# Kernel tuning notes

Hardware: AMD Instinct MI355X
Metric: run time of the kernel (lower is better)

## Reference

```python
import jax, jax.numpy as jnp
import numpy as np

WAY = 5
SHOT = 5
SCALE = 10.0
EPS = 1e-8


def setup_inputs() -> dict:
    key = jax.random.key(0)
    k1, k2 = jax.random.split(key, 2)
    x = jax.random.normal(k1, (100, 512, 16, 16), dtype=jnp.float32)
    W = jax.random.normal(k2, (512, 512), dtype=jnp.float32) * 0.02  # 1x1 conv weight (outC, inC)
    b = jnp.zeros((512,), dtype=jnp.float32)
    return {"x": x, "W": W, "b": b}


def reference(x, W, b):
    B, C, H, Wd = x.shape
    # extract(): 1x1 conv -> softmax over flattened (C*H*W) per sample -> remask
    mask = jnp.einsum('bchw,oc->bohw', x, W) + b[None, :, None, None]
    mask = jax.nn.softmax(mask.reshape(B, -1), axis=1).reshape(B, C, H, Wd)
    x = x * mask
    # predict(): (way, shot+query, C, H, W)
    xv = x.reshape(WAY, -1, C, H, Wd)
    s = xv[:, :SHOT].mean(axis=(1, 3, 4))                    # (m=way, d=C) support prototypes
    q = xv[:, SHOT:].reshape(-1, C, H * Wd)                  # (n, d=C, f=H*W) queries
    # cosine_similarity over d, without materializing (n,m,d,f)
    qn = jnp.maximum(jnp.sqrt(jnp.sum(q * q, axis=1)), EPS)  # (n, f)
    sn = jnp.maximum(jnp.sqrt(jnp.sum(s * s, axis=1)), EPS)  # (m,)
    scores = jnp.einsum('ndf,md->nmf', q, s) / (qn[:, None, :] * sn[None, :, None])
    # softmax over classes (m), then mean over spatial positions f
    return jax.nn.softmax(SCALE * scores, axis=1).mean(axis=2)  # (n, way)
```

## Files before the change

kernel.cpp:

```cpp
#include <hip/hip_runtime.h>
#include <hip/hip_bf16.h>
#include <math.h>

typedef _Float16 half8 __attribute__((ext_vector_type(8)));
typedef float f32x4 __attribute__((ext_vector_type(4)));

#define BATCH 100
#define CH    512
#define HWP   256
#define SAMP  (CH * HWP)

__device__ __forceinline__ void async16(const void* g, void* l) {
  __builtin_amdgcn_global_load_lds(
      (const __attribute__((address_space(1))) unsigned int*)g,
      (__attribute__((address_space(3))) unsigned int*)l, 16, 0, 0);
}

__global__ __launch_bounds__(256) void k_txpose(const float* __restrict__ x,
                                               _Float16* __restrict__ xh) {
  __shared__ float tb[64][69];
  int bid  = blockIdx.x;
  int b    = bid >> 5;
  int tile = bid & 31;
  int c0 = (tile >> 2) << 6;
  int p0 = (tile & 3) << 6;
  int t = threadIdx.x;
  const float* xb = x + (size_t)b * SAMP;
#pragma unroll
  for (int it = 0; it < 4; it++) {
    int ch = it * 256 + t;
    int c  = ch >> 4;
    int pc = (ch & 15) << 2;
    float4 v = *(const float4*)(xb + (size_t)(c0 + c) * HWP + p0 + pc);
    tb[c][pc] = v.x; tb[c][pc + 1] = v.y; tb[c][pc + 2] = v.z; tb[c][pc + 3] = v.w;
  }
  __syncthreads();
  _Float16* xhb = xh + (size_t)b * SAMP;
#pragma unroll
  for (int it = 0; it < 2; it++) {
    int ch = it * 256 + t;
    int p  = ch >> 3;
    int ck = (ch & 7) << 3;
    half8 h;
#pragma unroll
    for (int j = 0; j < 8; j++) h[j] = (_Float16)tb[ck + j][p];
    *(half8*)(xhb + (size_t)(p0 + p) * CH + c0 + ck) = h;
  }
}

__global__ __launch_bounds__(256) void k_convw(const float* __restrict__ W,
                                              _Float16* __restrict__ Wh) {
  int base = blockIdx.x * 1024 + threadIdx.x;
#pragma unroll
  for (int j = 0; j < 4; j++) Wh[base + j * 256] = (_Float16)W[base + j * 256];
}

__global__ __launch_bounds__(256) void k_gemm(const _Float16* __restrict__ Wh,
                                             const _Float16* __restrict__ xh,
                                             const float* __restrict__ bias,
                                             _Float16* __restrict__ u,
                                             float* __restrict__ denom) {
  __shared__ __align__(16) _Float16 smem[128 * 136];
  _Float16* As = smem;
  _Float16* Bs = smem + 4096;
  int bid   = blockIdx.x;
  int batch = bid >> 3;
  int sub   = bid & 7;
  int ot = sub & 3, pt = sub >> 2;
  int o0 = ot * 128, p0 = pt * 128;
  const _Float16* Bg = xh + (size_t)batch * SAMP;

  int t  = threadIdx.x;
  int wv = t >> 6, ln = t & 63;
  int qd = ln >> 4, r = ln & 15;
  int wm0 = (wv >> 1) * 64, wn0 = (wv & 1) * 64;

  f32x4 acc[4][4] = {};

  for (int kk = 0; kk < 512; kk += 32) {
#pragma unroll
    for (int it = 0; it < 2; it++) {
      int ch  = it * 256 + t;
      int row = ch >> 2;
      int qc  = ch & 3;
      char* la = (char*)As + (size_t)(it * 256 + wv * 64) * 16;
      char* lb = (char*)Bs + (size_t)(it * 256 + wv * 64) * 16;
      async16((const char*)(Wh + (size_t)(o0 + row) * 512 + kk + qc * 8), la);
      async16((const char*)(Bg + (size_t)(p0 + row) * 512 + kk + qc * 8), lb);
    }
    __syncthreads();
    half8 af[4], bf[4];
#pragma unroll
    for (int i = 0; i < 4; i++)
      af[i] = *(const half8*)(As + (wm0 + i * 16 + r) * 32 + qd * 8);
#pragma unroll
    for (int j = 0; j < 4; j++)
      bf[j] = *(const half8*)(Bs + (wn0 + j * 16 + r) * 32 + qd * 8);
#pragma unroll
    for (int i = 0; i < 4; i++)
#pragma unroll
      for (int j = 0; j < 4; j++)
        acc[i][j] = __builtin_amdgcn_mfma_f32_16x16x32_f16(af[i], bf[j], acc[i][j], 0, 0, 0);
    __syncthreads();
  }

#pragma unroll
  for (int it = 0; it < 8; it++) {
    int ch = it * 256 + t;
    int p  = ch >> 4;
    int ck = ch & 15;
    half8 v = *(const half8*)(Bg + (size_t)(p0 + p) * CH + o0 + ck * 8);
    *(half8*)(smem + p * 136 + ck * 8) = v;
  }
  __syncthreads();

  _Float16* outb = u + (size_t)batch * SAMP;
  float lsum = 0.f;
#pragma unroll
  for (int i = 0; i < 4; i++) {
#pragma unroll
    for (int rg = 0; rg < 4; rg++) {
      int ol = wm0 + i * 16 + qd * 4 + rg;
      float bv = bias[o0 + ol];
#pragma unroll
      for (int j = 0; j < 4; j++) {
        int pl = wn0 + j * 16 + r;
        float ev = __expf(acc[i][j][rg] + bv);
        lsum += ev;
        float xv = (float)smem[pl * 136 + ol];
        outb[(size_t)(o0 + ol) * HWP + p0 + pl] = (_Float16)(xv * ev);
      }
    }
  }
#pragma unroll
  for (int off = 32; off; off >>= 1) lsum += __shfl_down(lsum, off, 64);
  __shared__ float rs[4];
  if (ln == 0) rs[wv] = lsum;
  __syncthreads();
  if (t == 0) atomicAdd(&denom[batch], rs[0] + rs[1] + rs[2] + rs[3]);
}

__global__ __launch_bounds__(256) void k_proto(const _Float16* __restrict__ u,
                                              const float* __restrict__ denom,
                                              float* __restrict__ sproto) {
  int m = blockIdx.x / 512, c = blockIdx.x % 512;
  int t = threadIdx.x;
  float acc = 0.f;
  for (int j = 0; j < 5; j++) {
    int b = m * 20 + j;
    float invd = 1.0f / denom[b];
    acc += (float)u[(size_t)b * SAMP + (size_t)c * HWP + t] * invd;
  }
#pragma unroll
  for (int off = 32; off; off >>= 1) acc += __shfl_down(acc, off, 64);
  __shared__ float rs[4];
  if ((t & 63) == 0) rs[t >> 6] = acc;
  __syncthreads();
  if (t == 0) sproto[m * 512 + c] = (rs[0] + rs[1] + rs[2] + rs[3]) * (1.0f / 1280.0f);
}

__global__ __launch_bounds__(256) void k_sn(const float* __restrict__ sproto,
                                           float* __restrict__ pref) {
  int m = blockIdx.x, t = threadIdx.x;
  float v1 = sproto[m * 512 + t], v2 = sproto[m * 512 + 256 + t];
  float acc = v1 * v1 + v2 * v2;
#pragma unroll
  for (int off = 32; off; off >>= 1) acc += __shfl_down(acc, off, 64);
  __shared__ float rs[4];
  if ((t & 63) == 0) rs[t >> 6] = acc;
  __syncthreads();
  if (t == 0) {
    float sn = fmaxf(sqrtf(rs[0] + rs[1] + rs[2] + rs[3]), 1e-8f);
    pref[m] = 10.0f / sn;
  }
}

__global__ __launch_bounds__(256) void k_part(const _Float16* __restrict__ u,
                                             const float* __restrict__ sproto,
                                             float* __restrict__ part) {
  __shared__ float s_l[5 * 64];
  int n = blockIdx.x >> 3, gc = blockIdx.x & 7;
  int b = (n / 15) * 20 + 5 + (n % 15);
  int t = threadIdx.x;
  for (int i = t; i < 320; i += 256)
    s_l[i] = sproto[(i >> 6) * 512 + gc * 64 + (i & 63)];
  __syncthreads();
  const _Float16* ub = u + (size_t)b * SAMP + (size_t)gc * 64 * HWP;
  float dot[5] = {0, 0, 0, 0, 0}, qq = 0.f;
#pragma unroll 8
  for (int c = 0; c < 64; c++) {
    float v = (float)ub[c * HWP + t];
    qq += v * v;
#pragma unroll
    for (int m = 0; m < 5; m++) dot[m] += v * s_l[m * 64 + c];
  }
  float* pp = part + (((size_t)n * 8 + gc) * 256 + t) * 6;
  pp[0] = dot[0]; pp[1] = dot[1]; pp[2] = dot[2];
  pp[3] = dot[3]; pp[4] = dot[4]; pp[5] = qq;
}

__global__ __launch_bounds__(256) void k_comb(const float* __restrict__ part,
                                             const float* __restrict__ pref,
                                             float* __restrict__ out) {
  int n = blockIdx.x, t = threadIdx.x;
  float dot[5] = {0, 0, 0, 0, 0}, qq = 0.f;
#pragma unroll
  for (int gc = 0; gc < 8; gc++) {
    const float* pp = part + (((size_t)n * 8 + gc) * 256 + t) * 6;
    dot[0] += pp[0]; dot[1] += pp[1]; dot[2] += pp[2];
    dot[3] += pp[3]; dot[4] += pp[4]; qq += pp[5];
  }
  float iqn = 1.0f / fmaxf(sqrtf(qq), 1e-20f);
  float sc[5], mx = -1e30f;
#pragma unroll
  for (int m = 0; m < 5; m++) { sc[m] = dot[m] * pref[m] * iqn; mx = fmaxf(mx, sc[m]); }
  float p[5], ssum = 0.f;
#pragma unroll
  for (int m = 0; m < 5; m++) { p[m] = __expf(sc[m] - mx); ssum += p[m]; }
  float rr = 1.0f / ssum;
#pragma unroll
  for (int m = 0; m < 5; m++) {
    float v = p[m] * rr;
#pragma unroll
    for (int off = 32; off; off >>= 1) v += __shfl_down(v, off, 64);
    p[m] = v;
  }
  __shared__ float rs[4][5];
  if ((t & 63) == 0) {
#pragma unroll
    for (int m = 0; m < 5; m++) rs[t >> 6][m] = p[m];
  }
  __syncthreads();
  if (t < 5) out[n * 5 + t] =
      (rs[0][t] + rs[1][t] + rs[2][t] + rs[3][t]) * (1.0f / 256.0f);
}

extern "C" void kernel_launch(void* const* d_in, const int* in_sizes, int n_in,
                              void* d_out, int out_size, void* d_ws, size_t ws_size,
                              hipStream_t stream) {
  const float* x    = (const float*)d_in[0];
  const float* W    = (const float*)d_in[1];
  const float* bias = (const float*)d_in[2];
  float* out = (float*)d_out;

  char* ws = (char*)d_ws;
  _Float16* xh     = (_Float16*)(ws + 0);
  float*    part   = (float*)   (ws + 0);
  _Float16* Wh     = (_Float16*)(ws + 26214400);
  _Float16* u      = (_Float16*)(ws + 26738688);
  float*    denom  = (float*)   (ws + 52953088);
  float*    sproto = (float*)   (ws + 52953600);
  float*    pref   = (float*)   (ws + 52963840);

  hipMemsetAsync(denom, 0, 512, stream);
  k_txpose <<<3200, 256, 0, stream>>>(x, xh);
  k_convw  <<<256,  256, 0, stream>>>(W, Wh);
  k_gemm   <<<800,  256, 0, stream>>>(Wh, xh, bias, u, denom);
  k_proto  <<<2560, 256, 0, stream>>>(u, denom, sproto);
  k_sn     <<<5,    256, 0, stream>>>(sproto, pref);
  k_part   <<<600,  256, 0, stream>>>(u, sproto, part);
  k_comb   <<<75,   256, 0, stream>>>(part, pref, out);
}
```

Before: 142.1 us.

## Fuse small kernels and stage GEMM epilogue through LDS for coalesced stores

```diff
diff --git a/kernel.cpp b/kernel.cpp
--- a/kernel.cpp
+++ b/kernel.cpp
@@ -17,14 +17,22 @@
 }
 
 __global__ __launch_bounds__(256) void k_txpose(const float* __restrict__ x,
-                                               _Float16* __restrict__ xh) {
+                                               _Float16* __restrict__ xh,
+                                               const float* __restrict__ W,
+                                               _Float16* __restrict__ Wh) {
+  int bid = blockIdx.x;
+  int t = threadIdx.x;
+  if (bid >= 3200) {
+    int base = (bid - 3200) * 1024 + t;
+#pragma unroll
+    for (int j = 0; j < 4; j++) Wh[base + j * 256] = (_Float16)W[base + j * 256];
+    return;
+  }
   __shared__ float tb[64][69];
-  int bid  = blockIdx.x;
   int b    = bid >> 5;
   int tile = bid & 31;
   int c0 = (tile >> 2) << 6;
   int p0 = (tile & 3) << 6;
-  int t = threadIdx.x;
   const float* xb = x + (size_t)b * SAMP;
 #pragma unroll
   for (int it = 0; it < 4; it++) {
@@ -48,21 +56,15 @@
   }
 }
 
-__global__ __launch_bounds__(256) void k_convw(const float* __restrict__ W,
-                                              _Float16* __restrict__ Wh) {
-  int base = blockIdx.x * 1024 + threadIdx.x;
-#pragma unroll
-  for (int j = 0; j < 4; j++) Wh[base + j * 256] = (_Float16)W[base + j * 256];
-}
-
 __global__ __launch_bounds__(256) void k_gemm(const _Float16* __restrict__ Wh,
                                              const _Float16* __restrict__ xh,
                                              const float* __restrict__ bias,
                                              _Float16* __restrict__ u,
                                              float* __restrict__ denom) {
-  __shared__ __align__(16) _Float16 smem[128 * 136];
-  _Float16* As = smem;
-  _Float16* Bs = smem + 4096;
+  __shared__ __align__(16) _Float16 As[128 * 32];
+  __shared__ __align__(16) _Float16 Bs[128 * 32];
+  __shared__ __align__(16) _Float16 xk[128 * 136];
+  __shared__ float rs[4];
   int bid   = blockIdx.x;
   int batch = bid >> 3;
   int sub   = bid & 7;
@@ -88,6 +90,17 @@
       async16((const char*)(Wh + (size_t)(o0 + row) * 512 + kk + qc * 8), la);
       async16((const char*)(Bg + (size_t)(p0 + row) * 512 + kk + qc * 8), lb);
     }
+    if ((unsigned)(kk - o0) < 128u) {
+      int ko = kk - o0;
+#pragma unroll
+      for (int it = 0; it < 2; it++) {
+        int ch  = it * 256 + t;
+        int row = ch >> 2;
+        int qc  = ch & 3;
+        half8 v = *(const half8*)(Bg + (size_t)(p0 + row) * 512 + kk + qc * 8);
+        *(half8*)(xk + row * 136 + ko + qc * 8) = v;
+      }
+    }
     __syncthreads();
     half8 af[4], bf[4];
 #pragma unroll
@@ -104,17 +117,6 @@
     __syncthreads();
   }
 
-#pragma unroll
-  for (int it = 0; it < 8; it++) {
-    int ch = it * 256 + t;
-    int p  = ch >> 4;
-    int ck = ch & 15;
-    half8 v = *(const half8*)(Bg + (size_t)(p0 + p) * CH + o0 + ck * 8);
-    *(half8*)(smem + p * 136 + ck * 8) = v;
-  }
-  __syncthreads();
-
-  _Float16* outb = u + (size_t)batch * SAMP;
   float lsum = 0.f;
 #pragma unroll
   for (int i = 0; i < 4; i++) {
@@ -127,17 +129,38 @@
         int pl = wn0 + j * 16 + r;
         float ev = __expf(acc[i][j][rg] + bv);
         lsum += ev;
-        float xv = (float)smem[pl * 136 + ol];
-        outb[(size_t)(o0 + ol) * HWP + p0 + pl] = (_Float16)(xv * ev);
+        acc[i][j][rg] = (float)xk[pl * 136 + ol] * ev;
       }
     }
   }
 #pragma unroll
   for (int off = 32; off; off >>= 1) lsum += __shfl_down(lsum, off, 64);
-  __shared__ float rs[4];
   if (ln == 0) rs[wv] = lsum;
   __syncthreads();
   if (t == 0) atomicAdd(&denom[batch], rs[0] + rs[1] + rs[2] + rs[3]);
+
+#pragma unroll
+  for (int i = 0; i < 4; i++)
+#pragma unroll
+    for (int rg = 0; rg < 4; rg++) {
+      int ol = wm0 + i * 16 + qd * 4 + rg;
+#pragma unroll
+      for (int j = 0; j < 4; j++) {
+        int pl = wn0 + j * 16 + r;
+        xk[ol * 136 + pl] = (_Float16)acc[i][j][rg];
+      }
+    }
+  __syncthreads();
+
+  _Float16* outb = u + (size_t)batch * SAMP + (size_t)o0 * HWP + p0;
+#pragma unroll
+  for (int it = 0; it < 8; it++) {
+    int ch  = it * 256 + t;
+    int row = ch >> 4;
+    int ck  = ch & 15;
+    half8 v = *(const half8*)(xk + row * 136 + ck * 8);
+    *(half8*)(outb + (size_t)row * HWP + ck * 8) = v;
+  }
 }
 
 __global__ __launch_bounds__(256) void k_proto(const _Float16* __restrict__ u,
@@ -159,22 +182,6 @@
   if (t == 0) sproto[m * 512 + c] = (rs[0] + rs[1] + rs[2] + rs[3]) * (1.0f / 1280.0f);
 }
 
-__global__ __launch_bounds__(256) void k_sn(const float* __restrict__ sproto,
-                                           float* __restrict__ pref) {
-  int m = blockIdx.x, t = threadIdx.x;
-  float v1 = sproto[m * 512 + t], v2 = sproto[m * 512 + 256 + t];
-  float acc = v1 * v1 + v2 * v2;
-#pragma unroll
-  for (int off = 32; off; off >>= 1) acc += __shfl_down(acc, off, 64);
-  __shared__ float rs[4];
-  if ((t & 63) == 0) rs[t >> 6] = acc;
-  __syncthreads();
-  if (t == 0) {
-    float sn = fmaxf(sqrtf(rs[0] + rs[1] + rs[2] + rs[3]), 1e-8f);
-    pref[m] = 10.0f / sn;
-  }
-}
-
 __global__ __launch_bounds__(256) void k_part(const _Float16* __restrict__ u,
                                              const float* __restrict__ sproto,
                                              float* __restrict__ part) {
@@ -200,9 +207,19 @@
 }
 
 __global__ __launch_bounds__(256) void k_comb(const float* __restrict__ part,
-                                             const float* __restrict__ pref,
+                                             const float* __restrict__ sproto,
                                              float* __restrict__ out) {
+  __shared__ float prefs[5];
   int n = blockIdx.x, t = threadIdx.x;
+  int wvi = t >> 6, ln = t & 63;
+  for (int m = wvi; m < 5; m += 4) {
+    float a = 0.f;
+    for (int i = ln; i < 512; i += 64) { float v = sproto[m * 512 + i]; a += v * v; }
+#pragma unroll
+    for (int off = 32; off; off >>= 1) a += __shfl_down(a, off, 64);
+    if (ln == 0) prefs[m] = 10.0f / fmaxf(sqrtf(a), 1e-8f);
+  }
+  __syncthreads();
   float dot[5] = {0, 0, 0, 0, 0}, qq = 0.f;
 #pragma unroll
   for (int gc = 0; gc < 8; gc++) {
@@ -213,7 +230,7 @@
   float iqn = 1.0f / fmaxf(sqrtf(qq), 1e-20f);
   float sc[5], mx = -1e30f;
 #pragma unroll
-  for (int m = 0; m < 5; m++) { sc[m] = dot[m] * pref[m] * iqn; mx = fmaxf(mx, sc[m]); }
+  for (int m = 0; m < 5; m++) { sc[m] = dot[m] * prefs[m] * iqn; mx = fmaxf(mx, sc[m]); }
   float p[5], ssum = 0.f;
 #pragma unroll
   for (int m = 0; m < 5; m++) { p[m] = __expf(sc[m] - mx); ssum += p[m]; }
@@ -225,14 +242,14 @@
     for (int off = 32; off; off >>= 1) v += __shfl_down(v, off, 64);
     p[m] = v;
   }
-  __shared__ float rs[4][5];
-  if ((t & 63) == 0) {
-#pragma unroll
-    for (int m = 0; m < 5; m++) rs[t >> 6][m] = p[m];
+  __shared__ float rsb[4][5];
+  if (ln == 0) {
+#pragma unroll
+    for (int m = 0; m < 5; m++) rsb[wvi][m] = p[m];
   }
   __syncthreads();
   if (t < 5) out[n * 5 + t] =
-      (rs[0][t] + rs[1][t] + rs[2][t] + rs[3][t]) * (1.0f / 256.0f);
+      (rsb[0][t] + rsb[1][t] + rsb[2][t] + rsb[3][t]) * (1.0f / 256.0f);
 }
 
 extern "C" void kernel_launch(void* const* d_in, const int* in_sizes, int n_in,
@@ -250,14 +267,11 @@
   _Float16* u      = (_Float16*)(ws + 26738688);
   float*    denom  = (float*)   (ws + 52953088);
   float*    sproto = (float*)   (ws + 52953600);
-  float*    pref   = (float*)   (ws + 52963840);
 
   hipMemsetAsync(denom, 0, 512, stream);
-  k_txpose <<<3200, 256, 0, stream>>>(x, xh);
-  k_convw  <<<256,  256, 0, stream>>>(W, Wh);
+  k_txpose <<<3456, 256, 0, stream>>>(x, xh, W, Wh);
   k_gemm   <<<800,  256, 0, stream>>>(Wh, xh, bias, u, denom);
   k_proto  <<<2560, 256, 0, stream>>>(u, denom, sproto);
-  k_sn     <<<5,    256, 0, stream>>>(sproto, pref);
   k_part   <<<600,  256, 0, stream>>>(u, sproto, part);
-  k_comb   <<<75,   256, 0, stream>>>(part, pref, out);
-}
+  k_comb   <<<75,   256, 0, stream>>>(part, sproto, out);
+}
```

Result: no change. 143.4 us (+0.9%).
